# Performance work log

Measured on AMD Instinct MI355X. Metric: run time of the kernel, lower is better.

Reference implementation:

```python
import jax, jax.numpy as jnp
import numpy as np

B, S, D, H = 2, 2048, 1024, 16
DK = D // H


def setup_inputs() -> dict:
    key = jax.random.key(0)
    ks = jax.random.split(key, 12)
    scale = 1.0 / np.sqrt(D)
    inp = {
        "query": jax.random.normal(ks[0], (B, S, D), jnp.float32),
        "key": jax.random.normal(ks[1], (B, S, D), jnp.float32),
        "value": jax.random.normal(ks[2], (B, S, D), jnp.float32),
        "mask": jax.random.randint(ks[3], (B, 1, S, S), 0, 2, jnp.int32),
        "Wq": jax.random.normal(ks[4], (D, D), jnp.float32) * scale,
        "bq": jnp.zeros((D,), jnp.float32),
        "Wk": jax.random.normal(ks[5], (D, D), jnp.float32) * scale,
        "bk": jnp.zeros((D,), jnp.float32),
        "Wv": jax.random.normal(ks[6], (D, D), jnp.float32) * scale,
        "bv": jnp.zeros((D,), jnp.float32),
        "Wo": jax.random.normal(ks[7], (D, D), jnp.float32) * scale,
        "bo": jnp.zeros((D,), jnp.float32),
    }
    return inp


def reference(query, key, value, mask, Wq, bq, Wk, bk, Wv, bv, Wo, bo):
    # Linear projections (dropout is identity in eval mode)
    q = query @ Wq + bq          # (B,S,D)
    k = key @ Wk + bk
    v = value @ Wv + bv

    # split heads: (B,S,D) -> (B,H,S,DK)
    def split(x):
        return x.reshape(B, S, H, DK).transpose(0, 2, 1, 3)

    q, k, v = split(q), split(k), split(v)

    scores = jnp.einsum("bhqd,bhkd->bhqk", q, k) / jnp.sqrt(jnp.float32(DK))
    scores = jnp.where(mask == 0, jnp.float32(-1e9), scores)
    p_attn = jax.nn.softmax(scores, axis=-1)   # (B,H,S,S)

    att = jnp.einsum("bhqk,bhkd->bhqd", p_attn, v)  # (B,H,S,DK)
    merged = att.transpose(0, 2, 1, 3).reshape(B, S, D)
    return merged @ Wo + bo
```

## Files before the change

kernel.cpp:

```cpp
#include <hip/hip_runtime.h>
#include <hip/hip_bf16.h>
#include <cstdint>
#include <cstddef>


#define B_ 2
#define S_ 2048
#define D_ 1024
#define H_ 16
#define M_ 4096

typedef unsigned short u16;
typedef __attribute__((ext_vector_type(8))) short bf16x8;
typedef __attribute__((ext_vector_type(8))) unsigned short u16x8;
typedef __attribute__((ext_vector_type(4))) unsigned short u16x4;
typedef __attribute__((ext_vector_type(4))) unsigned int u32x4;
typedef __attribute__((ext_vector_type(4))) float f32x4;
typedef __attribute__((ext_vector_type(4))) int i32x4;

#define QSCALE 0.18033688011112042f

__device__ __forceinline__ u16 f2bf(float f) {
  __hip_bfloat16 h = __float2bfloat16(f);
  return *reinterpret_cast<u16*>(&h);
}

__device__ __forceinline__ unsigned cvtpk(float lo, float hi) {
  unsigned r;
  asm("v_cvt_pk_bf16_f32 %0, %1, %2" : "=v"(r) : "v"(lo), "v"(hi));
  return r;
}

__device__ __forceinline__ void gload_lds16(const void* g, void* l) {
  __builtin_amdgcn_global_load_lds((const __attribute__((address_space(1))) void*)g,
                                   (__attribute__((address_space(3))) void*)l, 16, 0, 0);
}

__global__ __launch_bounds__(256) void k_convert(const float* __restrict__ q, const float* __restrict__ k,
                                                 const float* __restrict__ v,
                                                 u16* __restrict__ xq, u16* __restrict__ xk, u16* __restrict__ xv) {
  int z = blockIdx.y;
  const float* src = (z == 0) ? q : (z == 1) ? k : v;
  u16* dst = (z == 0) ? xq : (z == 1) ? xk : xv;
  size_t i = ((size_t)blockIdx.x * 256 + threadIdx.x) * 8;
  f32x4 a = *(const f32x4*)(src + i);
  f32x4 b = *(const f32x4*)(src + i + 4);
  u16x8 o;
  o[0]=f2bf(a[0]); o[1]=f2bf(a[1]); o[2]=f2bf(a[2]); o[3]=f2bf(a[3]);
  o[4]=f2bf(b[0]); o[5]=f2bf(b[1]); o[6]=f2bf(b[2]); o[7]=f2bf(b[3]);
  *(u16x8*)(dst + i) = o;
}

__global__ __launch_bounds__(256) void k_transposeW(const float* __restrict__ w0, const float* __restrict__ w1,
                                                    const float* __restrict__ w2, const float* __restrict__ w3,
                                                    u16* __restrict__ t0, u16* __restrict__ t1,
                                                    u16* __restrict__ t2, u16* __restrict__ t3) {
  int z = blockIdx.z;
  const float* W = (z==0)?w0:(z==1)?w1:(z==2)?w2:w3;
  u16* Wt = (z==0)?t0:(z==1)?t1:(z==2)?t2:t3;
  __shared__ float tile[32][33];
  int tx = threadIdx.x & 31, ty = threadIdx.x >> 5;
  int bx = blockIdx.x * 32, by = blockIdx.y * 32;
  #pragma unroll
  for (int p = 0; p < 4; ++p)
    tile[ty + p*8][tx] = W[(size_t)(by + ty + p*8) * D_ + bx + tx];
  __syncthreads();
  #pragma unroll
  for (int p = 0; p < 4; ++p)
    Wt[(size_t)(bx + ty + p*8) * D_ + by + tx] = f2bf(tile[tx][ty + p*8]);
}

__global__ __launch_bounds__(256) void k_packmask(const int* __restrict__ mask, u16* __restrict__ out) {
  size_t t = (size_t)blockIdx.x * 256 + threadIdx.x;
  const int* p = mask + t * 64;
  unsigned wds0 = 0, wds1 = 0, wds2 = 0, wds3 = 0;
  #pragma unroll
  for (int c = 0; c < 16; ++c) {
    i32x4 v = *(const i32x4*)(p + c*4);
    #pragma unroll
    for (int e = 0; e < 4; ++e) {
      const int k = c*4 + e;
      const int lcw = (k >> 3) & 3;
      const int ni = ((k >> 4) & 2) | ((k >> 2) & 1);
      const unsigned bit = 1u << (4*ni + (k & 3));
      if (v[e]) {
        if (lcw == 0) wds0 |= bit; else if (lcw == 1) wds1 |= bit;
        else if (lcw == 2) wds2 |= bit; else wds3 |= bit;
      }
    }
  }
  u16x4 w; w[0] = (u16)wds0; w[1] = (u16)wds1; w[2] = (u16)wds2; w[3] = (u16)wds3;
  *(u16x4*)(out + t*4) = w;
}

template<int CMODE, int MI, int NI>
__device__ __forceinline__ void gemm_core(const u16* __restrict__ A, const u16* __restrict__ Bt,
                                          const float* __restrict__ bias, void* __restrict__ Cv, float scale) {
  extern __shared__ u16 sm[];
  constexpr int ASZ = MI*32*64;
  u16* As = sm;
  u16* Bs = sm + ASZ;
  const int t = threadIdx.x;
  const int l = t & 63, w = t >> 6;
  const int wr = w >> 1, wc = w & 1;
  const int lr = l & 15, lc = l >> 4;
  const int bm = blockIdx.x, bn = blockIdx.y;
  f32x4 acc[MI][NI];
  #pragma unroll
  for (int i = 0; i < MI; ++i)
    #pragma unroll
    for (int j = 0; j < NI; ++j) { f32x4 z = {0.f,0.f,0.f,0.f}; acc[i][j] = z; }
  const int srow = t >> 3;
  const int blkx = (t & 7) ^ (srow & 7);
  const u16* ga = A  + (size_t)(bm*(MI*32) + srow)*1024 + blkx*8;
  const u16* gb = Bt + (size_t)(bn*(NI*32) + srow)*1024 + blkx*8;
  for (int kt = 0; kt < 16; ++kt) {
    const int ko = kt * 64;
    __syncthreads();
    #pragma unroll
    for (int i = 0; i < MI; ++i)
      gload_lds16(ga + (size_t)(i*32)*1024 + ko, &As[i*2048 + t*8]);
    #pragma unroll
    for (int i = 0; i < NI; ++i)
      gload_lds16(gb + (size_t)(i*32)*1024 + ko, &Bs[i*2048 + t*8]);
    __syncthreads();
    #pragma unroll
    for (int ks = 0; ks < 2; ++ks) {
      bf16x8 af[MI], bfr[NI];
      #pragma unroll
      for (int mi = 0; mi < MI; ++mi)
        af[mi]  = *(const bf16x8*)&As[(wr*(MI*16) + mi*16 + lr)*64 + (((ks*4 + lc) ^ (lr & 7))*8)];
      #pragma unroll
      for (int ni = 0; ni < NI; ++ni)
        bfr[ni] = *(const bf16x8*)&Bs[(wc*(NI*16) + ni*16 + lr)*64 + (((ks*4 + lc) ^ (lr & 7))*8)];
      #pragma unroll
      for (int mi = 0; mi < MI; ++mi)
        #pragma unroll
        for (int ni = 0; ni < NI; ++ni)
          acc[mi][ni] = __builtin_amdgcn_mfma_f32_16x16x32_bf16(af[mi], bfr[ni], acc[mi][ni], 0, 0, 0);
    }
  }
  #pragma unroll
  for (int ni = 0; ni < NI; ++ni) {
    int gcol = bn*(NI*32) + wc*(NI*16) + ni*16 + lr;
    float bv = bias[gcol];
    #pragma unroll
    for (int mi = 0; mi < MI; ++mi) {
      int grow = bm*(MI*32) + wr*(MI*16) + mi*16 + lc*4;
      if (CMODE == 2) {
        u16x4 pk;
        #pragma unroll
        for (int j = 0; j < 4; ++j) pk[j] = f2bf((acc[mi][ni][j] + bv) * scale);
        *(u16x4*)&((u16*)Cv)[(size_t)gcol * M_ + grow] = pk;
      } else {
        #pragma unroll
        for (int j = 0; j < 4; ++j) {
          float v = (acc[mi][ni][j] + bv) * scale;
          if (CMODE == 0) ((u16*)Cv)[(size_t)(grow + j) * 1024 + gcol] = f2bf(v);
          else            ((float*)Cv)[(size_t)(grow + j) * 1024 + gcol] = v;
        }
      }
    }
  }
}

__global__ __launch_bounds__(256, 4) void k_gemm_qkv(const u16* Xq, const u16* Xk, const u16* Xv,
                                                     const u16* Wqt, const u16* Wkt, const u16* Wvt,
                                                     const float* bq, const float* bk, const float* bv,
                                                     u16* Qo, u16* Ko, u16* Vt, float qscale) {
  int z = blockIdx.z;
  if (z == 0)      gemm_core<0,4,4>(Xq, Wqt, bq, Qo, qscale);
  else if (z == 1) gemm_core<0,4,4>(Xk, Wkt, bk, Ko, 1.f);
  else             gemm_core<2,4,4>(Xv, Wvt, bv, Vt, 1.f);
}

__global__ __launch_bounds__(256, 4) void k_gemm_out(const u16* Aatt, const u16* Wot, const float* bo, float* out) {
  gemm_core<1,4,2>(Aatt, Wot, bo, out, 1.f);
}

__global__ __launch_bounds__(256) void k_attn(const u16* __restrict__ Q, const u16* __restrict__ Kb,
                                              const u16* __restrict__ Vt,
                                              const u16* __restrict__ mbw,
                                              u16* __restrict__ attb) {
  __shared__ u16 Ks[3*4096];
  __shared__ u16 Vs[2*4096];
  const int t = threadIdx.x, l = t & 63, w = t >> 6;
  const int lr = l & 15, lc = l >> 4;
  const int id = blockIdx.x + (blockIdx.y << 5) + (blockIdx.z << 9);
  const int lg = (id & 7) * 128 + (id >> 3);
  const int qt = lg & 31, h = (lg >> 5) & 15, b = lg >> 9;
  const int r0 = t >> 3;
  const int c0 = (t & 7) ^ (r0 & 7);
  const int pr0 = ((r0 & 12) << 1) | ((r0 & 16) >> 2) | (r0 & 3);
  const u16* kp0 = Kb + (size_t)(b*S_ + pr0)*D_ + h*64 + c0*8;
  const u16* vp0 = Vt + (size_t)(h*64 + r0)*M_ + b*S_ + c0*8;

  gload_lds16(Q + (size_t)(b*S_ + qt*64 + r0)*D_      + h*64 + c0*8, &Ks[t*8]);
  gload_lds16(Q + (size_t)(b*S_ + qt*64 + r0 + 32)*D_ + h*64 + c0*8, &Ks[2048 + t*8]);
  __syncthreads();
  const int qrow = w*16 + lr;
  const int sw0 = ((lc     ) ^ (lr & 7)) * 8;
  const int sw1 = ((4 + lc ) ^ (lr & 7)) * 8;
  bf16x8 aq0 = *(const bf16x8*)&Ks[qrow*64 + sw0];
  bf16x8 aq1 = *(const bf16x8*)&Ks[qrow*64 + sw1];
  __syncthreads();
  gload_lds16(kp0,                                 &Ks[t*8]);
  gload_lds16(kp0 + (size_t)32*D_,                 &Ks[2048 + t*8]);
  gload_lds16(vp0,                                 &Vs[t*8]);
  gload_lds16(vp0 + (size_t)32*M_,                 &Vs[2048 + t*8]);
  gload_lds16(kp0 + (size_t)64*D_,                 &Ks[4096 + t*8]);
  gload_lds16(kp0 + (size_t)64*D_ + (size_t)32*D_, &Ks[4096 + 2048 + t*8]);

  const short one_bf = (short)0x3F80;
  const bf16x8 onesf = {one_bf,one_bf,one_bf,one_bf,one_bf,one_bf,one_bf,one_bf};
  f32x4 ls = {0.f,0.f,0.f,0.f};
  f32x4 o[4];
  #pragma unroll
  for (int ni = 0; ni < 4; ++ni) { f32x4 z = {0.f,0.f,0.f,0.f}; o[ni] = z; }
  const u16* mkp = mbw + (size_t)(b*S_ + qt*64 + qrow)*128 + lc;
  const u16* vpA = vp0;
  const u16* vpB = vp0 + (size_t)32*M_;
  const u16* kpA = kp0;
  const u16* kpB = kp0 + (size_t)32*D_;

#define AITER(N, KC, VC, VN, KNN, KPRE, VPRE, WAITN) {                                 \
    asm volatile("s_waitcnt vmcnt(" #WAITN ")");                                       \
    __builtin_amdgcn_s_barrier();                                                      \
    __builtin_amdgcn_sched_barrier(0);                                                 \
    unsigned mw = mkp[(N)*4];                                                          \
    if (VPRE) {                                                                        \
      gload_lds16(vpA + ((N)+1)*64, &Vs[(VN)*4096 + t*8]);                             \
      gload_lds16(vpB + ((N)+1)*64, &Vs[(VN)*4096 + 2048 + t*8]);                      \
    }                                                                                  \
    if (KPRE) {                                                                        \
      gload_lds16(kpA + (size_t)((N)+2)*64*D_, &Ks[(KNN)*4096 + t*8]);                 \
      gload_lds16(kpB + (size_t)((N)+2)*64*D_, &Ks[(KNN)*4096 + 2048 + t*8]);          \
    }                                                                                  \
    f32x4 s[4];                                                                        \
    _Pragma("unroll")                                                                  \
    for (int ni = 0; ni < 4; ++ni) { f32x4 z = {0.f,0.f,0.f,0.f}; s[ni] = z; }         \
    __builtin_amdgcn_s_setprio(1);                                                     \
    _Pragma("unroll")                                                                  \
    for (int ni = 0; ni < 4; ++ni) {                                                   \
      bf16x8 bk0 = *(const bf16x8*)&Ks[(KC)*4096 + (ni*16 + lr)*64 + sw0];             \
      bf16x8 bk1 = *(const bf16x8*)&Ks[(KC)*4096 + (ni*16 + lr)*64 + sw1];             \
      s[ni] = __builtin_amdgcn_mfma_f32_16x16x32_bf16(bk0, aq0, s[ni], 0, 0, 0);       \
      s[ni] = __builtin_amdgcn_mfma_f32_16x16x32_bf16(bk1, aq1, s[ni], 0, 0, 0);       \
    }                                                                                  \
    __builtin_amdgcn_s_setprio(0);                                                     \
    _Pragma("unroll")                                                                  \
    for (int ni = 0; ni < 4; ++ni)                                                     \
      _Pragma("unroll")                                                                \
      for (int j = 0; j < 4; ++j) {                                                    \
        float pv = __builtin_amdgcn_exp2f(s[ni][j]);                                   \
        int bmsk = ((int)(mw << (31 - (4*ni + j)))) >> 31;                             \
        union { float f; int i; } u; u.f = pv; u.i &= bmsk;                            \
        s[ni][j] = u.f;                                                                \
      }                                                                                \
    u32x4 pw0, pw1;                                                                    \
    pw0[0] = cvtpk(s[0][0], s[0][1]); pw0[1] = cvtpk(s[0][2], s[0][3]);                \
    pw0[2] = cvtpk(s[1][0], s[1][1]); pw0[3] = cvtpk(s[1][2], s[1][3]);                \
    pw1[0] = cvtpk(s[2][0], s[2][1]); pw1[1] = cvtpk(s[2][2], s[2][3]);                \
    pw1[2] = cvtpk(s[3][0], s[3][1]); pw1[3] = cvtpk(s[3][2], s[3][3]);                \
    bf16x8 pa0 = __builtin_bit_cast(bf16x8, pw0);                                      \
    bf16x8 pa1 = __builtin_bit_cast(bf16x8, pw1);                                      \
    __builtin_amdgcn_s_setprio(1);                                                     \
    ls = __builtin_amdgcn_mfma_f32_16x16x32_bf16(pa0, onesf, ls, 0, 0, 0);             \
    ls = __builtin_amdgcn_mfma_f32_16x16x32_bf16(pa1, onesf, ls, 0, 0, 0);             \
    _Pragma("unroll")                                                                  \
    for (int ni = 0; ni < 4; ++ni) {                                                   \
      bf16x8 bv0 = *(const bf16x8*)&Vs[(VC)*4096 + (ni*16 + lr)*64 + sw0];             \
      o[ni] = __builtin_amdgcn_mfma_f32_16x16x32_bf16(pa0, bv0, o[ni], 0, 0, 0);       \
    }                                                                                  \
    _Pragma("unroll")                                                                  \
    for (int ni = 0; ni < 4; ++ni) {                                                   \
      bf16x8 bv1 = *(const bf16x8*)&Vs[(VC)*4096 + (ni*16 + lr)*64 + sw1];             \
      o[ni] = __builtin_amdgcn_mfma_f32_16x16x32_bf16(pa1, bv1, o[ni], 0, 0, 0);       \
    }                                                                                  \
    __builtin_amdgcn_s_setprio(0);                                                     \
  }

  for (int it = 0; it < 5; ++it) {
    AITER(0, 0,0, 1,2, 1,1, 2);
    AITER(1, 1,1, 0,0, 1,1, 2);
    AITER(2, 2,0, 1,1, 1,1, 2);
    AITER(3, 0,1, 0,2, 1,1, 2);
    AITER(4, 1,0, 1,0, 1,1, 2);
    AITER(5, 2,1, 0,1, 1,1, 2);
    mkp += 24;
    vpA += 6*64;            vpB += 6*64;
    kpA += (size_t)6*64*D_; kpB += (size_t)6*64*D_;
  }
  AITER(0, 0,0, 1,0, 0,1, 2);
  AITER(1, 1,1, 0,0, 0,0, 0);
#undef AITER

  float rl[4];
  #pragma unroll
  for (int j = 0; j < 4; ++j) rl[j] = 1.f / ls[j];
  #pragma unroll
  for (int ni = 0; ni < 4; ++ni)
    #pragma unroll
    for (int j = 0; j < 4; ++j) {
      int orow = qt*64 + w*16 + lc*4 + j, dcol = ni*16 + lr;
      attb[(size_t)(b*S_ + orow)*D_ + h*64 + dcol] = f2bf(o[ni][j] * rl[j]);
    }
}

extern "C" void kernel_launch(void* const* d_in, const int* in_sizes, int n_in,
                              void* d_out, int out_size, void* d_ws, size_t ws_size,
                              hipStream_t stream) {
  (void)in_sizes; (void)n_in; (void)out_size; (void)ws_size;
  const float* query = (const float*)d_in[0];
  const float* key   = (const float*)d_in[1];
  const float* value = (const float*)d_in[2];
  const int*   mask  = (const int*)d_in[3];
  const float* Wq = (const float*)d_in[4];
  const float* bq = (const float*)d_in[5];
  const float* Wk = (const float*)d_in[6];
  const float* bk = (const float*)d_in[7];
  const float* Wv = (const float*)d_in[8];
  const float* bv = (const float*)d_in[9];
  const float* Wo = (const float*)d_in[10];
  const float* bo = (const float*)d_in[11];
  float* out = (float*)d_out;
  char* ws = (char*)d_ws;
  const size_t MB = 1024 * 1024;
  u16* Xq  = (u16*)(ws + 0*MB);
  u16* Xk  = (u16*)(ws + 8*MB);
  u16* Xv  = (u16*)(ws + 16*MB);
  u16* Wqt = (u16*)(ws + 24*MB);
  u16* Wkt = (u16*)(ws + 26*MB);
  u16* Wvt = (u16*)(ws + 28*MB);
  u16* Wot = (u16*)(ws + 30*MB);
  u16* Qb  = (u16*)(ws + 32*MB);
  u16* Kb  = (u16*)(ws + 40*MB);
  u16* Vtb = (u16*)(ws + 48*MB);
  u16* mbits = (u16*)(ws + 56*MB);
  u16* attb = (u16*)(ws + 0*MB);

  k_convert  <<<dim3(2048, 3),     256, 0,     stream>>>(query, key, value, Xq, Xk, Xv);
  k_transposeW<<<dim3(32, 32, 4),  256, 0,     stream>>>(Wq, Wk, Wv, Wo, Wqt, Wkt, Wvt, Wot);
  k_packmask <<<dim3(512),         256, 0,     stream>>>(mask, mbits);
  k_gemm_qkv <<<dim3(32, 8, 3),    256, 32768, stream>>>(Xq, Xk, Xv, Wqt, Wkt, Wvt, bq, bk, bv,
                                                         Qb, Kb, Vtb, QSCALE);
  k_attn     <<<dim3(32, 16, 2),   256, 0,     stream>>>(Qb, Kb, Vtb, mbits, attb);
  k_gemm_out <<<dim3(32, 16),      256, 24576, stream>>>(attb, Wot, bo, out);
}
```

Baseline: 136.5 us.

## Double attention query tile to 128 rows with 512-thread blocks sharing K/V tiles

Result: faster. 131.4 us, median of 2 (-3.8%).

```diff
diff --git a/kernel.cpp b/kernel.cpp
--- a/kernel.cpp
+++ b/kernel.cpp
@@ -178,38 +178,36 @@
   gemm_core<1,4,2>(Aatt, Wot, bo, out, 1.f);
 }
 
-__global__ __launch_bounds__(256) void k_attn(const u16* __restrict__ Q, const u16* __restrict__ Kb,
-                                              const u16* __restrict__ Vt,
-                                              const u16* __restrict__ mbw,
-                                              u16* __restrict__ attb) {
+__global__ __launch_bounds__(512, 4) void k_attn(const u16* __restrict__ Q, const u16* __restrict__ Kb,
+                                                 const u16* __restrict__ Vt,
+                                                 const u16* __restrict__ mbw,
+                                                 u16* __restrict__ attb) {
   __shared__ u16 Ks[3*4096];
   __shared__ u16 Vs[2*4096];
   const int t = threadIdx.x, l = t & 63, w = t >> 6;
   const int lr = l & 15, lc = l >> 4;
-  const int id = blockIdx.x + (blockIdx.y << 5) + (blockIdx.z << 9);
-  const int lg = (id & 7) * 128 + (id >> 3);
-  const int qt = lg & 31, h = (lg >> 5) & 15, b = lg >> 9;
+  const int id = blockIdx.x + (blockIdx.y << 4) + (blockIdx.z << 8);
+  const int lg = (id & 7) * 64 + (id >> 3);
+  const int qt = lg & 15, h = (lg >> 4) & 15, b = lg >> 8;
   const int r0 = t >> 3;
   const int c0 = (t & 7) ^ (r0 & 7);
-  const int pr0 = ((r0 & 12) << 1) | ((r0 & 16) >> 2) | (r0 & 3);
+  const int pr0 = (r0 & 32) | ((r0 & 12) << 1) | ((r0 & 16) >> 2) | (r0 & 3);
   const u16* kp0 = Kb + (size_t)(b*S_ + pr0)*D_ + h*64 + c0*8;
   const u16* vp0 = Vt + (size_t)(h*64 + r0)*M_ + b*S_ + c0*8;
 
-  gload_lds16(Q + (size_t)(b*S_ + qt*64 + r0)*D_      + h*64 + c0*8, &Ks[t*8]);
-  gload_lds16(Q + (size_t)(b*S_ + qt*64 + r0 + 32)*D_ + h*64 + c0*8, &Ks[2048 + t*8]);
+  gload_lds16(Q + (size_t)(b*S_ + qt*128 + r0)*D_      + h*64 + c0*8, &Ks[t*8]);
+  gload_lds16(Q + (size_t)(b*S_ + qt*128 + 64 + r0)*D_ + h*64 + c0*8, &Ks[4096 + t*8]);
   __syncthreads();
   const int qrow = w*16 + lr;
   const int sw0 = ((lc     ) ^ (lr & 7)) * 8;
   const int sw1 = ((4 + lc ) ^ (lr & 7)) * 8;
-  bf16x8 aq0 = *(const bf16x8*)&Ks[qrow*64 + sw0];
-  bf16x8 aq1 = *(const bf16x8*)&Ks[qrow*64 + sw1];
+  const int qbuf = (qrow >> 6) * 4096, qrl = (qrow & 63) * 64;
+  bf16x8 aq0 = *(const bf16x8*)&Ks[qbuf + qrl + sw0];
+  bf16x8 aq1 = *(const bf16x8*)&Ks[qbuf + qrl + sw1];
   __syncthreads();
-  gload_lds16(kp0,                                 &Ks[t*8]);
-  gload_lds16(kp0 + (size_t)32*D_,                 &Ks[2048 + t*8]);
-  gload_lds16(vp0,                                 &Vs[t*8]);
-  gload_lds16(vp0 + (size_t)32*M_,                 &Vs[2048 + t*8]);
-  gload_lds16(kp0 + (size_t)64*D_,                 &Ks[4096 + t*8]);
-  gload_lds16(kp0 + (size_t)64*D_ + (size_t)32*D_, &Ks[4096 + 2048 + t*8]);
+  gload_lds16(kp0,                  &Ks[t*8]);
+  gload_lds16(vp0,                  &Vs[t*8]);
+  gload_lds16(kp0 + (size_t)64*D_,  &Ks[4096 + t*8]);
 
   const short one_bf = (short)0x3F80;
   const bf16x8 onesf = {one_bf,one_bf,one_bf,one_bf,one_bf,one_bf,one_bf,one_bf};
@@ -217,25 +215,17 @@
   f32x4 o[4];
   #pragma unroll
   for (int ni = 0; ni < 4; ++ni) { f32x4 z = {0.f,0.f,0.f,0.f}; o[ni] = z; }
-  const u16* mkp = mbw + (size_t)(b*S_ + qt*64 + qrow)*128 + lc;
+  const u16* mkp = mbw + (size_t)(b*S_ + qt*128 + qrow)*128 + lc;
   const u16* vpA = vp0;
-  const u16* vpB = vp0 + (size_t)32*M_;
   const u16* kpA = kp0;
-  const u16* kpB = kp0 + (size_t)32*D_;
 
 #define AITER(N, KC, VC, VN, KNN, KPRE, VPRE, WAITN) {                                 \
     asm volatile("s_waitcnt vmcnt(" #WAITN ")");                                       \
     __builtin_amdgcn_s_barrier();                                                      \
     __builtin_amdgcn_sched_barrier(0);                                                 \
     unsigned mw = mkp[(N)*4];                                                          \
-    if (VPRE) {                                                                        \
-      gload_lds16(vpA + ((N)+1)*64, &Vs[(VN)*4096 + t*8]);                             \
-      gload_lds16(vpB + ((N)+1)*64, &Vs[(VN)*4096 + 2048 + t*8]);                      \
-    }                                                                                  \
-    if (KPRE) {                                                                        \
-      gload_lds16(kpA + (size_t)((N)+2)*64*D_, &Ks[(KNN)*4096 + t*8]);                 \
-      gload_lds16(kpB + (size_t)((N)+2)*64*D_, &Ks[(KNN)*4096 + 2048 + t*8]);          \
-    }                                                                                  \
+    if (VPRE) gload_lds16(vpA + ((N)+1)*64,              &Vs[(VN)*4096 + t*8]);        \
+    if (KPRE) gload_lds16(kpA + (size_t)((N)+2)*64*D_,   &Ks[(KNN)*4096 + t*8]);       \
     f32x4 s[4];                                                                        \
     _Pragma("unroll")                                                                  \
     for (int ni = 0; ni < 4; ++ni) { f32x4 z = {0.f,0.f,0.f,0.f}; s[ni] = z; }         \
@@ -281,17 +271,17 @@
   }
 
   for (int it = 0; it < 5; ++it) {
-    AITER(0, 0,0, 1,2, 1,1, 2);
-    AITER(1, 1,1, 0,0, 1,1, 2);
-    AITER(2, 2,0, 1,1, 1,1, 2);
-    AITER(3, 0,1, 0,2, 1,1, 2);
-    AITER(4, 1,0, 1,0, 1,1, 2);
-    AITER(5, 2,1, 0,1, 1,1, 2);
+    AITER(0, 0,0, 1,2, 1,1, 1);
+    AITER(1, 1,1, 0,0, 1,1, 1);
+    AITER(2, 2,0, 1,1, 1,1, 1);
+    AITER(3, 0,1, 0,2, 1,1, 1);
+    AITER(4, 1,0, 1,0, 1,1, 1);
+    AITER(5, 2,1, 0,1, 1,1, 1);
     mkp += 24;
-    vpA += 6*64;            vpB += 6*64;
-    kpA += (size_t)6*64*D_; kpB += (size_t)6*64*D_;
-  }
-  AITER(0, 0,0, 1,0, 0,1, 2);
+    vpA += 6*64;
+    kpA += (size_t)6*64*D_;
+  }
+  AITER(0, 0,0, 1,0, 0,1, 1);
   AITER(1, 1,1, 0,0, 0,0, 0);
 #undef AITER
 
@@ -302,7 +292,7 @@
   for (int ni = 0; ni < 4; ++ni)
     #pragma unroll
     for (int j = 0; j < 4; ++j) {
-      int orow = qt*64 + w*16 + lc*4 + j, dcol = ni*16 + lr;
+      int orow = qt*128 + w*16 + lc*4 + j, dcol = ni*16 + lr;
       attb[(size_t)(b*S_ + orow)*D_ + h*64 + dcol] = f2bf(o[ni][j] * rl[j]);
     }
 }
@@ -344,6 +334,6 @@
   k_packmask <<<dim3(512),         256, 0,     stream>>>(mask, mbits);
   k_gemm_qkv <<<dim3(32, 8, 3),    256, 32768, stream>>>(Xq, Xk, Xv, Wqt, Wkt, Wvt, bq, bk, bv,
                                                          Qb, Kb, Vtb, QSCALE);
-  k_attn     <<<dim3(32, 16, 2),   256, 0,     stream>>>(Qb, Kb, Vtb, mbits, attb);
+  k_attn     <<<dim3(16, 16, 2),   512, 0,     stream>>>(Qb, Kb, Vtb, mbits, attb);
   k_gemm_out <<<dim3(32, 16),      256, 24576, stream>>>(attb, Wot, bo, out);
 }
```
